# Kernel optimization log

Hardware: AMD Instinct MI355X
Metric: run time of the kernel (lower is better)

The kernel has to match this reference:

```python
import jax, jax.numpy as jnp
import numpy as np

MASK_FILL = -1e9
LN_EPS = 1e-5


def setup_inputs() -> dict:
    key = jax.random.key(0)
    ks = jax.random.split(key, 8)
    b, n, d = 4, 4096, 768
    k, ds = 64, 32
    x = jax.random.normal(ks[0], (b, n, d), dtype=jnp.float32)
    encoded_descriptions = jax.random.normal(ks[1], (k, ds, d), dtype=jnp.float32)
    description_attention_mask = jax.random.randint(ks[2], (k, ds), 0, 2).astype(jnp.int32)
    attention_masks = jax.random.randint(ks[3], (b, n), 0, 2).astype(jnp.int32)
    std = 0.03
    Wk = std * jax.random.normal(ks[4], (d, d), dtype=jnp.float32)
    Wv = std * jax.random.normal(ks[5], (d, d), dtype=jnp.float32)
    Wo = std * jax.random.normal(ks[6], (1, d), dtype=jnp.float32)
    bo = jnp.zeros((1,), dtype=jnp.float32)
    ln_gamma = jnp.ones((d,), dtype=jnp.float32)
    ln_beta = jnp.zeros((d,), dtype=jnp.float32)
    return {
        "x": x,
        "encoded_descriptions": encoded_descriptions,
        "description_attention_mask": description_attention_mask,
        "attention_masks": attention_masks,
        "Wk": Wk, "Wv": Wv, "Wo": Wo, "bo": bo,
        "ln_gamma": ln_gamma, "ln_beta": ln_beta,
    }


def reference(x, encoded_descriptions, description_attention_mask, attention_masks,
              Wk, Wv, Wo, bo, ln_gamma, ln_beta):
    # x: [b, n, d]; encoded_descriptions: [k, ds, d]
    d = x.shape[-1]
    scale = 1.0 / jnp.sqrt(jnp.float32(d))

    k_note = jnp.einsum('bni,oi->bno', x, Wk)  # nn.Linear: x @ W.T
    v_note = jnp.einsum('bni,oi->bno', x, Wv)

    # att: [b, k, ds, n]  (torch computes kdbn then permutes to bkdn)
    att = jnp.einsum('kdi,bni->bkdn', encoded_descriptions, k_note) * scale

    desc_mask = description_attention_mask.astype(bool)          # [k, ds]
    note_mask = attention_masks.astype(bool)                     # [b, n]
    combined = desc_mask[None, :, :, None] & note_mask[:, None, None, :]  # [b,k,ds,n]

    att = jnp.where(combined, att, MASK_FILL)
    attention = jax.nn.softmax(att, axis=-1)                     # [b,k,ds,n]

    context = jnp.einsum('bkdn,bni->bkdi', attention, v_note)    # [b,k,ds,d]

    desc_importance = attention.sum(axis=-1)                     # [b,k,ds]
    desc_importance = jnp.where(desc_mask[None, :, :], desc_importance, MASK_FILL)
    desc_weights = jax.nn.softmax(desc_importance, axis=-1)      # [b,k,ds]

    pooled = (context * desc_weights[..., None]).sum(axis=2)     # [b,k,d]

    mu = pooled.mean(axis=-1, keepdims=True)
    var = pooled.var(axis=-1, keepdims=True)
    y = (pooled - mu) * jax.lax.rsqrt(var + LN_EPS) * ln_gamma + ln_beta

    out = jnp.einsum('bkd,od->bko', y, Wo) + bo                  # [b,k,1]
    return out[..., 0]                                           # [b,k]
```

## Files before the change

kernel.cpp:

```cpp
#include <hip/hip_runtime.h>
#include <hip/hip_bf16.h>
#include <hip/hip_fp16.h>

typedef _Float16 half8 __attribute__((ext_vector_type(8)));
typedef _Float16 half4 __attribute__((ext_vector_type(4)));
typedef _Float16 half2v __attribute__((ext_vector_type(2)));
typedef float f32x4 __attribute__((ext_vector_type(4)));

#define LN_EPS 1e-5f
#define MASK_FILL -1e9f

__device__ __forceinline__ void async16(void* lds, const void* g) {
  __builtin_amdgcn_global_load_lds(
      (__attribute__((address_space(1))) void*)(g),
      (__attribute__((address_space(3))) void*)(lds), 16, 0, 0);
}

__global__ __launch_bounds__(256) void prep_all_kernel(
    const int* __restrict__ dmask, const int* __restrict__ amask,
    int* __restrict__ rowmap, float* __restrict__ row_w,
    int* __restrict__ start, int* __restrict__ keepM,
    int* __restrict__ perm, int* __restrict__ cntN) {
  __shared__ int lsum[256];
  __shared__ int nvs[64];
  const int tid = threadIdx.x;
  if (blockIdx.x == 0) {
    int flags[8];
    int cnt = 0;
#pragma unroll
    for (int u = 0; u < 8; u++) {
      flags[u] = dmask[tid * 8 + u] != 0;
      cnt += flags[u];
    }
    if (tid < 64) {
      int c = 0;
      for (int u = 0; u < 32; u++) c += (dmask[tid * 32 + u] != 0);
      nvs[tid] = c;
    }
    lsum[tid] = cnt;
    __syncthreads();
    for (int ofs = 1; ofs < 256; ofs <<= 1) {
      int t = (tid >= ofs) ? lsum[tid - ofs] : 0;
      __syncthreads();
      lsum[tid] += t;
      __syncthreads();
    }
    int excl = lsum[tid] - cnt;
    int pos = excl;
#pragma unroll
    for (int u = 0; u < 8; u++) {
      if (flags[u]) {
        int row = tid * 8 + u;
        rowmap[pos] = row;
        row_w[pos] = 1.0f / (float)nvs[row >> 5];
        pos++;
      }
    }
    if ((tid & 3) == 0) start[tid >> 2] = excl;
    if (tid == 255) {
      start[64] = lsum[255];
      *keepM = lsum[255];
    }
  } else {
    const int b = blockIdx.x - 1;
    const int* am = amask + (size_t)b * 4096;
    int flags[16];
    int cnt = 0;
#pragma unroll
    for (int u = 0; u < 16; u++) {
      flags[u] = am[tid * 16 + u] != 0;
      cnt += flags[u];
    }
    lsum[tid] = cnt;
    __syncthreads();
    for (int ofs = 1; ofs < 256; ofs <<= 1) {
      int t = (tid >= ofs) ? lsum[tid - ofs] : 0;
      __syncthreads();
      lsum[tid] += t;
      __syncthreads();
    }
    const int total = lsum[255];
    int vpos = lsum[tid] - cnt;
    int ipos = total + (tid * 16 - vpos);
    int* pm = perm + (size_t)b * 4096;
#pragma unroll
    for (int u = 0; u < 16; u++) {
      int g = tid * 16 + u;
      if (flags[u]) pm[vpos++] = g;
      else pm[ipos++] = g;
    }
    if (tid == 0) cntN[b] = total;
  }
}

__global__ __launch_bounds__(256) void gather_cast_all_kernel(
    const float* __restrict__ x, const float* __restrict__ enc,
    const float* __restrict__ Wv, const float* __restrict__ Wk,
    const int* __restrict__ perm, const int* __restrict__ rowmap,
    const int* __restrict__ keepM,
    _Float16* __restrict__ xh_c, _Float16* __restrict__ enc_c,
    _Float16* __restrict__ wvh, _Float16* __restrict__ wkT) {
  __shared__ float tile[32][33];
  const int bid = blockIdx.x;
  const int t = threadIdx.x;
  if (bid < 16384) {
    const int b = bid >> 12, ci = bid & 4095;
    const int n = perm[(size_t)b * 4096 + ci];
    const float* s = x + ((size_t)b * 4096 + n) * 768;
    _Float16* d = xh_c + ((size_t)b * 4096 + ci) * 768;
#pragma unroll
    for (int u = 0; u < 3; u++) d[t + u * 256] = (_Float16)s[t + u * 256];
  } else if (bid < 18432) {
    const int r = bid - 16384;
    _Float16* d = enc_c + (size_t)r * 768;
    if (r < *keepM) {
      const float* s = enc + (size_t)rowmap[r] * 768;
#pragma unroll
      for (int u = 0; u < 3; u++) d[t + u * 256] = (_Float16)s[t + u * 256];
    } else {
      int* di = (int*)d;
      for (int i = t; i < 384; i += 256) di[i] = 0;
    }
  } else if (bid < 19008) {
    const int base = (bid - 18432) * 1024 + t * 4;
    float4 v = *(const float4*)(Wv + base);
    half4 h = { (_Float16)v.x, (_Float16)v.y, (_Float16)v.z, (_Float16)v.w };
    *(half4*)(wvh + base) = h;
  } else {
    const int tb = bid - 19008;
    const int bc = (tb % 24) * 32, br = (tb / 24) * 32;
    const int lc = t & 31, lr0 = t >> 5;
    for (int i = lr0; i < 32; i += 8)
      tile[i][lc] = Wk[(size_t)(br + i) * 768 + bc + lc];
    __syncthreads();
    for (int i = lr0; i < 32; i += 8)
      wkT[(size_t)(bc + i) * 768 + br + lc] = (_Float16)tile[lc][i];
  }
}

template<bool OUT_F32, bool XCD>
__global__ __launch_bounds__(256) void gemm_f16_kernel(
    const _Float16* __restrict__ A, const _Float16* __restrict__ Bt,
    void* __restrict__ C, int M, int N, int K, float alpha,
    size_t strideBt, size_t strideC, const int* __restrict__ keepRows,
    const int* __restrict__ keepN) {
  int bx = blockIdx.x, by = blockIdx.y, bz = blockIdx.z;
  if (XCD) {
    const int gx = gridDim.x, gy = gridDim.y;
    const int total = gx * gy * gridDim.z;
    const int L = bx + gx * (by + gy * bz);
    const int orig = (L & 7) * (total >> 3) + (L >> 3);
    bx = orig % gx;
    const int rest = orig / gx;
    by = rest % gy;
    bz = rest / gy;
  }
  const int bm = bx * 64, bn = by * 128;
  if (keepRows && bm >= *keepRows) return;
  if (keepN && bn >= keepN[bz]) return;
  __shared__ _Float16 As[64 * 64];
  __shared__ _Float16 Bs[128 * 64];
  const int tid = threadIdx.x;
  const size_t z = bz;
  const int wave = tid >> 6, lane = tid & 63;
  const int wr = (wave >> 1) * 32, wc = (wave & 1) * 64;
  const int fr = lane & 15, xr = lane & 7;
  f32x4 acc[2][4] = {};
  const int lrow = lane >> 3;
  const int scol = (((lane & 7) ^ lrow)) * 8;
  const _Float16* ga = A + (size_t)(bm + wave * 16 + lrow) * K + scol;
  const _Float16* gb = Bt + z * strideBt + (size_t)(bn + wave * 32 + lrow) * K + scol;
  _Float16* lA = &As[(wave * 16) * 64];
  _Float16* lB = &Bs[(wave * 32) * 64];
  for (int k0 = 0; k0 < K; k0 += 64) {
    __syncthreads();
#pragma unroll
    for (int i = 0; i < 2; i++)
      async16(lA + i * 8 * 64, ga + (size_t)(8 * i) * K + k0);
#pragma unroll
    for (int i = 0; i < 4; i++)
      async16(lB + i * 8 * 64, gb + (size_t)(8 * i) * K + k0);
    __syncthreads();
#pragma unroll
    for (int k2 = 0; k2 < 2; k2++) {
      const int sb = k2 * 4 + (lane >> 4);
      const int so = (sb ^ xr) * 8;
      half8 af[2], bf[4];
#pragma unroll
      for (int i = 0; i < 2; i++)
        af[i] = *(const half8*)&As[(wr + i * 16 + fr) * 64 + so];
#pragma unroll
      for (int j = 0; j < 4; j++)
        bf[j] = *(const half8*)&Bs[(wc + j * 16 + fr) * 64 + so];
#pragma unroll
      for (int i = 0; i < 2; i++)
#pragma unroll
        for (int j = 0; j < 4; j++)
          acc[i][j] = __builtin_amdgcn_mfma_f32_16x16x32_f16(af[i], bf[j], acc[i][j], 0, 0, 0);
    }
  }
  const int rg = (lane >> 4) * 4;
#pragma unroll
  for (int i = 0; i < 2; i++) {
#pragma unroll
    for (int j = 0; j < 4; j++) {
      int col = bn + wc + j * 16 + fr;
#pragma unroll
      for (int r = 0; r < 4; r++) {
        int row = bm + wr + i * 16 + rg + r;
        float v = acc[i][j][r] * alpha;
        if (OUT_F32)
          ((float*)C)[z * strideC + (size_t)row * N + col] = v;
        else
          ((_Float16*)C)[z * strideC + (size_t)row * N + col] = (_Float16)v;
      }
    }
  }
}

__device__ __forceinline__ float block_reduce(float v, bool do_max, float* wbuf, int tid) {
#pragma unroll
  for (int m = 32; m; m >>= 1) {
    float o = __shfl_xor(v, m);
    v = do_max ? fmaxf(v, o) : (v + o);
  }
  if ((tid & 63) == 0) wbuf[tid >> 6] = v;
  __syncthreads();
  float r = do_max ? fmaxf(fmaxf(wbuf[0], wbuf[1]), fmaxf(wbuf[2], wbuf[3]))
                   : (wbuf[0] + wbuf[1] + wbuf[2] + wbuf[3]);
  __syncthreads();
  return r;
}

__global__ __launch_bounds__(256) void row_stats_kernel(
    const _Float16* __restrict__ S, const float* __restrict__ row_w,
    const int* __restrict__ keepM, const int* __restrict__ cntN,
    float4* __restrict__ stats_c) {
  const int r = blockIdx.x;
  if (r >= *keepM) return;
  __shared__ float wbuf[4];
  const int b = blockIdx.z;
  const int tid = threadIdx.x;
  const int cnt = cntN[b];
  if (cnt == 0) return;
  const float w = row_w[r];
  const int c0 = tid * 16;
  const _Float16* sp = S + ((size_t)b * 2048 + r) * 4096 + c0;
  float a[16];
#pragma unroll
  for (int c = 0; c < 16; c++) a[c] = MASK_FILL;
  if (c0 < cnt) {
    half8 v0 = *(const half8*)(sp);
#pragma unroll
    for (int u = 0; u < 8; u++)
      if (c0 + u < cnt) a[u] = (float)v0[u];
    if (c0 + 8 < cnt) {
      half8 v1 = *(const half8*)(sp + 8);
#pragma unroll
      for (int u = 0; u < 8; u++)
        if (c0 + 8 + u < cnt) a[8 + u] = (float)v1[u];
    }
  }
  float mx = a[0];
#pragma unroll
  for (int c = 1; c < 16; c++) mx = fmaxf(mx, a[c]);
  mx = block_reduce(mx, true, wbuf, tid);
  float ls = 0.f;
#pragma unroll
  for (int c = 0; c < 16; c++) ls += expf(a[c] - mx);
  float denom = block_reduce(ls, false, wbuf, tid);
  if (tid == 0)
    stats_c[(size_t)b * 2048 + r] = make_float4(mx, w / denom, 0.f, 0.f);
}

__global__ __launch_bounds__(256) void combine_kernel(
    const _Float16* __restrict__ S, const float4* __restrict__ stats_c,
    const int* __restrict__ start, const int* __restrict__ cntN,
    float* __restrict__ ca) {
  const int kd = blockIdx.x;
  const int b = blockIdx.z;
  const int i = blockIdx.y * 512 + threadIdx.x * 2;
  const int i0 = start[kd], i1 = start[kd + 1];
  const int cnt = cntN[b];
  float acc0, acc1;
  if (i0 == i1 || cnt == 0) {
    acc0 = acc1 = 1.0f / 4096.0f;
  } else if (i >= cnt) {
    acc0 = acc1 = 0.f;
  } else {
    acc0 = 0.f;
    acc1 = 0.f;
    const _Float16* sp = S + ((size_t)b * 2048 + i0) * 4096 + i;
    for (int r = i0; r < i1; r++, sp += 4096) {
      float4 s4 = stats_c[(size_t)b * 2048 + r];
      half2v v = *(const half2v*)sp;
      acc0 += s4.y * expf((float)v[0] - s4.x);
      acc1 += s4.y * expf((float)v[1] - s4.x);
    }
    if (i + 1 >= cnt) acc1 = 0.f;
  }
  float2 rr = {acc0, acc1};
  *(float2*)&ca[((size_t)b * 64 + kd) * 4096 + i] = rr;
}

__global__ __launch_bounds__(256) void t_partial_kernel(
    const float* __restrict__ ca,
    const _Float16* __restrict__ xh,
    float* __restrict__ t_part) {
  __shared__ float casT[64][68];
  __shared__ float xs[64][132];
  const int jt = blockIdx.x;
  const int nc = blockIdx.y;
  const int b = blockIdx.z;
  const int tid = threadIdx.x;
  const int tm = tid >> 4, tj = tid & 15;
  const int r = tid >> 2;
  const int cg = (tid & 3) * 16;
  const int cc = (tid & 3) * 32;
  float acc[4][8] = {};
  for (int n0 = nc * 256; n0 < nc * 256 + 256; n0 += 64) {
    __syncthreads();
    const float* cap = ca + (size_t)(b * 64 + r) * 4096 + n0 + cg;
#pragma unroll
    for (int u = 0; u < 16; u += 4) {
      float4 c4 = *(const float4*)(cap + u);
      casT[cg + u][r] = c4.x;
      casT[cg + u + 1][r] = c4.y;
      casT[cg + u + 2][r] = c4.z;
      casT[cg + u + 3][r] = c4.w;
    }
    const _Float16* xp = xh + ((size_t)b * 4096 + n0 + r) * 768 + jt * 128 + cc;
#pragma unroll
    for (int u = 0; u < 32; u += 8) {
      half8 hv = *(const half8*)(xp + u);
      float4 w0 = {(float)hv[0], (float)hv[1], (float)hv[2], (float)hv[3]};
      float4 w1 = {(float)hv[4], (float)hv[5], (float)hv[6], (float)hv[7]};
      *(float4*)&xs[r][cc + u] = w0;
      *(float4*)&xs[r][cc + u + 4] = w1;
    }
    __syncthreads();
#pragma unroll 8
    for (int nn = 0; nn < 64; ++nn) {
      float4 cm = *(const float4*)&casT[nn][tm * 4];
      float4 xa = *(const float4*)&xs[nn][tj * 8];
      float4 xb = *(const float4*)&xs[nn][tj * 8 + 4];
      float cmv[4] = {cm.x, cm.y, cm.z, cm.w};
      float xjv[8] = {xa.x, xa.y, xa.z, xa.w, xb.x, xb.y, xb.z, xb.w};
#pragma unroll
      for (int i = 0; i < 4; i++)
#pragma unroll
        for (int j = 0; j < 8; j++) acc[i][j] += cmv[i] * xjv[j];
    }
  }
#pragma unroll
  for (int i = 0; i < 4; i++)
#pragma unroll
    for (int j = 0; j < 8; j++)
      t_part[((size_t)nc * 256 + b * 64 + tm * 4 + i) * 768 + jt * 128 + tj * 8 + j] = acc[i][j];
}

__global__ __launch_bounds__(256) void t_reduce_kernel(
    const float* __restrict__ t_part, _Float16* __restrict__ th) {
  int i = blockIdx.x * 256 + threadIdx.x;
  float s = 0.f;
#pragma unroll
  for (int nc = 0; nc < 16; ++nc) s += t_part[(size_t)nc * 196608 + i];
  th[i] = (_Float16)s;
}

__global__ __launch_bounds__(256) void ln_out_kernel(
    const float* __restrict__ pooled, const float* __restrict__ Wo,
    const float* __restrict__ bo, const float* __restrict__ gamma,
    const float* __restrict__ beta, float* __restrict__ out) {
  __shared__ float wbuf[4];
  const int row = blockIdx.x, tid = threadIdx.x;
  float p[3];
#pragma unroll
  for (int u = 0; u < 3; u++) p[u] = pooled[(size_t)row * 768 + tid + u * 256];
  float s1 = p[0] + p[1] + p[2];
  float s2 = p[0] * p[0] + p[1] * p[1] + p[2] * p[2];
  s1 = block_reduce(s1, false, wbuf, tid);
  s2 = block_reduce(s2, false, wbuf, tid);
  float mean = s1 * (1.f / 768.f);
  float var = s2 * (1.f / 768.f) - mean * mean;
  float rstd = rsqrtf(var + LN_EPS);
  float accv = 0.f;
#pragma unroll
  for (int u = 0; u < 3; u++) {
    int i = tid + u * 256;
    float y = (p[u] - mean) * rstd * gamma[i] + beta[i];
    accv += y * Wo[i];
  }
  accv = block_reduce(accv, false, wbuf, tid);
  if (tid == 0) out[row] = accv + bo[0];
}

extern "C" void kernel_launch(void* const* d_in, const int* in_sizes, int n_in,
                              void* d_out, int out_size, void* d_ws, size_t ws_size,
                              hipStream_t stream) {
  const float* x = (const float*)d_in[0];
  const float* enc = (const float*)d_in[1];
  const int* dmask = (const int*)d_in[2];
  const int* amask = (const int*)d_in[3];
  const float* Wk = (const float*)d_in[4];
  const float* Wv = (const float*)d_in[5];
  const float* Wo = (const float*)d_in[6];
  const float* bo = (const float*)d_in[7];
  const float* gamma = (const float*)d_in[8];
  const float* beta = (const float*)d_in[9];
  float* out = (float*)d_out;

  char* ws = (char*)d_ws;
  size_t off = 0;
  auto alloc = [&](size_t bytes) -> char* {
    char* p = ws + off;
    off += (bytes + 255) & ~((size_t)255);
    return p;
  };
  _Float16* xh_c = (_Float16*)alloc((size_t)16384 * 768 * 2);
  _Float16* wkT = (_Float16*)alloc((size_t)768 * 768 * 2);
  _Float16* wvh = (_Float16*)alloc((size_t)768 * 768 * 2);
  _Float16* enc_c = (_Float16*)alloc((size_t)2048 * 768 * 2);
  _Float16* encK_c = (_Float16*)alloc((size_t)2048 * 768 * 2);
  float* ca = (float*)alloc((size_t)4 * 64 * 4096 * 4);
  float* t_part = (float*)alloc((size_t)16 * 256 * 768 * 4);
  _Float16* th = (_Float16*)alloc((size_t)256 * 768 * 2);
  float* pooled = (float*)alloc((size_t)256 * 768 * 4);
  float4* stats_c = (float4*)alloc((size_t)4 * 2048 * 16);
  int* rowmap = (int*)alloc(2048 * 4);
  float* row_w = (float*)alloc(2048 * 4);
  int* start = (int*)alloc(65 * 4);
  int* keepM = (int*)alloc(4);
  int* perm = (int*)alloc((size_t)4 * 4096 * 4);
  int* cntN = (int*)alloc(4 * 4);

  const size_t s_one = (size_t)2048 * 4096 * 2;
  const bool batched = (off + 4 * s_one) <= ws_size;
  _Float16* S = (_Float16*)alloc(batched ? 4 * s_one : s_one);

  const float scale = 0.036084391824351615f;

  prep_all_kernel<<<5, 256, 0, stream>>>(
      dmask, amask, rowmap, row_w, start, keepM, perm, cntN);
  gather_cast_all_kernel<<<19584, 256, 0, stream>>>(
      x, enc, Wv, Wk, perm, rowmap, keepM, xh_c, enc_c, wvh, wkT);

  gemm_f16_kernel<false, false><<<dim3(32, 6), 256, 0, stream>>>(
      enc_c, wkT, encK_c, 2048, 768, 768, 1.0f, 0, 0, keepM, nullptr);

  if (batched) {
    gemm_f16_kernel<false, true><<<dim3(32, 32, 4), 256, 0, stream>>>(
        encK_c, xh_c, S, 2048, 4096, 768, scale,
        (size_t)4096 * 768, (size_t)2048 * 4096, keepM, cntN);
    row_stats_kernel<<<dim3(2048, 1, 4), 256, 0, stream>>>(
        S, row_w, keepM, cntN, stats_c);
    combine_kernel<<<dim3(64, 8, 4), 256, 0, stream>>>(
        S, stats_c, start, cntN, ca);
  } else {
    for (int b = 0; b < 4; b++) {
      gemm_f16_kernel<false, true><<<dim3(32, 32), 256, 0, stream>>>(
          encK_c, xh_c + (size_t)b * 4096 * 768, S, 2048, 4096, 768, scale,
          0, 0, keepM, cntN + b);
      row_stats_kernel<<<dim3(2048, 1, 1), 256, 0, stream>>>(
          S, row_w, keepM, cntN + b, stats_c + (size_t)b * 2048);
      combine_kernel<<<dim3(64, 8, 1), 256, 0, stream>>>(
          S, stats_c + (size_t)b * 2048, start, cntN + b,
          ca + (size_t)b * 64 * 4096);
    }
  }

  t_partial_kernel<<<dim3(6, 16, 4), 256, 0, stream>>>(ca, xh_c, t_part);
  t_reduce_kernel<<<768, 256, 0, stream>>>(t_part, th);
  gemm_f16_kernel<true, false><<<dim3(4, 6), 256, 0, stream>>>(
      th, wvh, pooled, 256, 768, 768, 1.0f, 0, 0, nullptr, nullptr);
  ln_out_kernel<<<256, 256, 0, stream>>>(pooled, Wo, bo, gamma, beta, out);
}
```

Before: 143.1 us.

## Fuse partial reduce, Wv projection and layernorm output into one tail kernel

Replaces the t_reduce, small fp16 GEMM and ln_out kernels with a single kernel per output row. Each block sums the 16 partials into LDS, computes the 768 projected values with a scalar dot product against the fp16 Wv rows, then applies layernorm and the output projection. This removes two launches and the intermediate th/pooled global round trips. In exchange, the matrix product runs on scalar ALUs instead of matrix cores, and every block rereads the full Wv with strided per-thread row access.

```diff
diff --git a/kernel.cpp b/kernel.cpp
--- a/kernel.cpp
+++ b/kernel.cpp
@@ -359,24 +359,39 @@
       t_part[((size_t)nc * 256 + b * 64 + tm * 4 + i) * 768 + jt * 128 + tj * 8 + j] = acc[i][j];
 }
 
-__global__ __launch_bounds__(256) void t_reduce_kernel(
-    const float* __restrict__ t_part, _Float16* __restrict__ th) {
-  int i = blockIdx.x * 256 + threadIdx.x;
-  float s = 0.f;
-#pragma unroll
-  for (int nc = 0; nc < 16; ++nc) s += t_part[(size_t)nc * 196608 + i];
-  th[i] = (_Float16)s;
-}
-
-__global__ __launch_bounds__(256) void ln_out_kernel(
-    const float* __restrict__ pooled, const float* __restrict__ Wo,
-    const float* __restrict__ bo, const float* __restrict__ gamma,
-    const float* __restrict__ beta, float* __restrict__ out) {
+__global__ __launch_bounds__(256) void tail_fused_kernel(
+    const float* __restrict__ t_part, const _Float16* __restrict__ wvh,
+    const float* __restrict__ Wo, const float* __restrict__ bo,
+    const float* __restrict__ gamma, const float* __restrict__ beta,
+    float* __restrict__ out) {
+  __shared__ float tld[768];
   __shared__ float wbuf[4];
-  const int row = blockIdx.x, tid = threadIdx.x;
+  const int row = blockIdx.x;
+  const int tid = threadIdx.x;
+#pragma unroll
+  for (int u = 0; u < 3; u++) {
+    const int j = tid + u * 256;
+    float s = 0.f;
+#pragma unroll
+    for (int nc = 0; nc < 16; nc++)
+      s += t_part[((size_t)nc * 256 + row) * 768 + j];
+    tld[j] = s;
+  }
+  __syncthreads();
   float p[3];
 #pragma unroll
-  for (int u = 0; u < 3; u++) p[u] = pooled[(size_t)row * 768 + tid + u * 256];
+  for (int u = 0; u < 3; u++) {
+    const int o = tid + u * 256;
+    const _Float16* wr = wvh + (size_t)o * 768;
+    float acc = 0.f;
+    for (int j = 0; j < 768; j += 8) {
+      half8 wv8 = *(const half8*)(wr + j);
+      const float* tj = &tld[j];
+#pragma unroll
+      for (int q = 0; q < 8; q++) acc += tj[q] * (float)wv8[q];
+    }
+    p[u] = acc;
+  }
   float s1 = p[0] + p[1] + p[2];
   float s2 = p[0] * p[0] + p[1] * p[1] + p[2] * p[2];
   s1 = block_reduce(s1, false, wbuf, tid);
@@ -424,8 +439,6 @@
   _Float16* encK_c = (_Float16*)alloc((size_t)2048 * 768 * 2);
   float* ca = (float*)alloc((size_t)4 * 64 * 4096 * 4);
   float* t_part = (float*)alloc((size_t)16 * 256 * 768 * 4);
-  _Float16* th = (_Float16*)alloc((size_t)256 * 768 * 2);
-  float* pooled = (float*)alloc((size_t)256 * 768 * 4);
   float4* stats_c = (float4*)alloc((size_t)4 * 2048 * 16);
   int* rowmap = (int*)alloc(2048 * 4);
   float* row_w = (float*)alloc(2048 * 4);
@@ -470,8 +483,6 @@
   }
 
   t_partial_kernel<<<dim3(6, 16, 4), 256, 0, stream>>>(ca, xh_c, t_part);
-  t_reduce_kernel<<<768, 256, 0, stream>>>(t_part, th);
-  gemm_f16_kernel<true, false><<<dim3(4, 6), 256, 0, stream>>>(
-      th, wvh, pooled, 256, 768, 768, 1.0f, 0, 0, nullptr, nullptr);
-  ln_out_kernel<<<256, 256, 0, stream>>>(pooled, Wo, bo, gamma, beta, out);
-}
+  tail_fused_kernel<<<256, 256, 0, stream>>>(
+      t_part, wvh, Wo, bo, gamma, beta, out);
+}
```

Result: slower. 164.4 us (+14.9%).
